# Performance work log

Measured on AMD Instinct MI355X. Metric: run time of the kernel, lower is better.

The kernel has to match this reference:

```python
import jax, jax.numpy as jnp
import numpy as np

SINKHORN_ITERS = 8
TEMPERATURE = 1.0
EPS = 1e-6


def sinkhorn(t):
    # log-domain Sinkhorn normalization, matching torch: log(clamp(t, min=eps)) / temp
    t = jnp.log(jnp.clip(t, EPS)) / TEMPERATURE
    for _ in range(SINKHORN_ITERS):
        t = t - jax.nn.logsumexp(t, axis=-2, keepdims=True)  # over tokens n
        t = t - jax.nn.logsumexp(t, axis=-1, keepdims=True)  # over experts e
    return jnp.exp(t)


def setup_inputs() -> dict:
    key = jax.random.key(0)
    k1, k2, k3 = jax.random.split(key, 3)
    B, N, D, E = 4, 4096, 1024, 8
    x = jax.random.normal(k1, (B, N, D), dtype=jnp.float32)
    gate_w = jax.random.normal(k2, (D, E), dtype=jnp.float32) * (D ** -0.5)
    experts = jax.random.normal(k3, (E, D, D), dtype=jnp.float32) * (D ** -0.5)
    return {"x": x, "gate_w": gate_w, "experts": experts}


def reference(x, gate_w, experts):
    B, N, D = x.shape
    E = gate_w.shape[-1]
    M = N // E  # tokens per expert

    gate_logits = jnp.einsum('bnd,de->bne', x, gate_w)
    competitive_gates = sinkhorn(gate_logits)  # b n e

    # topk along token dim (-2): transpose to (b,e,n), top_k along last axis
    vals, idx = jax.lax.top_k(jnp.swapaxes(competitive_gates, -1, -2), M)  # b e m
    gate_values = jnp.swapaxes(vals, -1, -2)   # b m e
    routed_indices = jnp.swapaxes(idx, -1, -2)  # b m e (int32)

    b_idx = jnp.arange(B)[:, None, None]  # (b,1,1)
    routed = x[b_idx, routed_indices]     # b m e d
    routed = jnp.transpose(routed, (2, 0, 1, 3))  # e b m d

    outputs = jnp.einsum('ebmd,edf->ebmf', routed, experts)  # e b m d
    outputs = outputs * jnp.transpose(gate_values, (2, 0, 1))[..., None]  # * (e b m 1)

    vals_bmed = jnp.transpose(outputs, (1, 2, 0, 3))  # b m e d
    routed_back = jnp.zeros_like(x).at[b_idx, routed_indices].set(vals_bmed)
    return routed_back
```

## Files before the change

kernel.cpp:

```cpp
#include <hip/hip_runtime.h>
#include <hip/hip_bf16.h>
#include <stdint.h>

typedef short s16x8 __attribute__((ext_vector_type(8)));
typedef float f32x4 __attribute__((ext_vector_type(4)));
typedef unsigned short u16;
typedef unsigned int u32;
typedef unsigned long long u64;

__device__ __forceinline__ float bf2f(u16 v){
  union { u32 u; float f; } c; c.u = ((u32)v) << 16; return c.f;
}

__device__ __forceinline__ u16 f2bf(float f){
  u32 u = __float_as_uint(f);
  u32 r = (u + 0x7FFFu + ((u >> 16) & 1u)) >> 16;
  return (u16)r;
}

__device__ __forceinline__ uint4 pack8(float4 a, float4 b){
  union { uint4 v; u16 s[8]; } o;
  o.s[0]=f2bf(a.x); o.s[1]=f2bf(a.y); o.s[2]=f2bf(a.z); o.s[3]=f2bf(a.w);
  o.s[4]=f2bf(b.x); o.s[5]=f2bf(b.y); o.s[6]=f2bf(b.z); o.s[7]=f2bf(b.w);
  return o.v;
}

__device__ __forceinline__ void gll16(const u16* g, u16* l){
  __builtin_amdgcn_global_load_lds((const __attribute__((address_space(1))) u32*)g,
                                   (__attribute__((address_space(3))) u32*)l, 16, 0, 0);
}

__global__ __launch_bounds__(64) void k_detect(const u32* __restrict__ x, int* __restrict__ flag){
  int lane = threadIdx.x;
  int cnt = 0;
  for (int i = lane; i < 4096; i += 64){
    u32 w = x[i];
    int ex = (w >> 7) & 0xFF;
    cnt += (ex >= 140) ? 1 : 0;
  }
  #pragma unroll
  for (int off = 32; off; off >>= 1) cnt += __shfl_xor(cnt, off, 64);
  if (lane == 0) *flag = (cnt > 256) ? 1 : 0;
}

__global__ __launch_bounds__(1024) void k_logits_cvt(const void* __restrict__ xv,
                                                     const void* __restrict__ gwv,
                                                     const int* __restrict__ flag,
                                                     u16* __restrict__ xb,
                                                     float* __restrict__ gates,
                                                     int mode){
  __shared__ float4 gw_swz[2048];
  __shared__ float  wacc[16][8];
  int is_f32 = *flag;
  int tid = threadIdx.x;

  {
    int r = tid;
    float g0,g1,g2,g3,g4,g5,g6,g7;
    if (is_f32){
      const float* gw = (const float*)gwv + ((size_t)r << 3);
      float4 u = *(const float4*)gw;
      float4 v = *(const float4*)(gw + 4);
      g0=u.x; g1=u.y; g2=u.z; g3=u.w; g4=v.x; g5=v.y; g6=v.z; g7=v.w;
    } else {
      union { uint4 v; u16 s[8]; } wu;
      wu.v = *(const uint4*)((const u16*)gwv + ((size_t)r << 3));
      g0=bf2f(wu.s[0]); g1=bf2f(wu.s[1]); g2=bf2f(wu.s[2]); g3=bf2f(wu.s[3]);
      g4=bf2f(wu.s[4]); g5=bf2f(wu.s[5]); g6=bf2f(wu.s[6]); g7=bf2f(wu.s[7]);
    }
    int p = r >> 3, j = r & 7;
    gw_swz[(p << 4) + (((j << 1)    ) ^ (p & 15))] = make_float4(g0,g1,g2,g3);
    gw_swz[(p << 4) + (((j << 1) | 1) ^ (p & 15))] = make_float4(g4,g5,g6,g7);
  }

  int tl = tid >> 7, pos = tid & 127;
  size_t base = ((((size_t)blockIdx.x << 3) + tl) << 10) + ((size_t)pos << 3);
  float xf[8];
  if (is_f32){
    const float* xr = (const float*)xv + base;
    float4 u = *(const float4*)xr;
    float4 v = *(const float4*)(xr + 4);
    xf[0]=u.x; xf[1]=u.y; xf[2]=u.z; xf[3]=u.w;
    xf[4]=v.x; xf[5]=v.y; xf[6]=v.z; xf[7]=v.w;
    if (mode) *(uint4*)(xb + base) = pack8(u, v);
  } else {
    uint4 raw = *(const uint4*)((const u16*)xv + base);
    union { uint4 v; u16 s[8]; } xu; xu.v = raw;
    #pragma unroll
    for (int k = 0; k < 8; k++) xf[k] = bf2f(xu.s[k]);
    if (mode) *(uint4*)(xb + base) = raw;
  }
  __syncthreads();

  float a0=0,a1=0,a2=0,a3=0,a4=0,a5=0,a6=0,a7=0;
  #pragma unroll
  for (int j = 0; j < 8; j++){
    float4 wA = gw_swz[(pos << 4) + (((j << 1)    ) ^ (pos & 15))];
    float4 wB = gw_swz[(pos << 4) + (((j << 1) | 1) ^ (pos & 15))];
    float xv8 = xf[j];
    a0 += xv8*wA.x; a1 += xv8*wA.y; a2 += xv8*wA.z; a3 += xv8*wA.w;
    a4 += xv8*wB.x; a5 += xv8*wB.y; a6 += xv8*wB.z; a7 += xv8*wB.w;
  }
  int wave = tid >> 6, lane = tid & 63;
  int s1 = lane & 1;
  float k0 = s1 ? a4 : a0, g0 = s1 ? a0 : a4;
  float k1 = s1 ? a5 : a1, g1 = s1 ? a1 : a5;
  float k2 = s1 ? a6 : a2, g2 = s1 ? a2 : a6;
  float k3 = s1 ? a7 : a3, g3 = s1 ? a3 : a7;
  k0 += __shfl_xor(g0, 1, 64); k1 += __shfl_xor(g1, 1, 64);
  k2 += __shfl_xor(g2, 1, 64); k3 += __shfl_xor(g3, 1, 64);
  int s2 = (lane >> 1) & 1;
  float m0 = s2 ? k2 : k0, h0 = s2 ? k0 : k2;
  float m1 = s2 ? k3 : k1, h1 = s2 ? k1 : k3;
  m0 += __shfl_xor(h0, 2, 64); m1 += __shfl_xor(h1, 2, 64);
  int s3 = (lane >> 2) & 1;
  float r = s3 ? m1 : m0, h = s3 ? m0 : m1;
  r += __shfl_xor(h, 4, 64);
  r += __shfl_xor(r, 8, 64);
  r += __shfl_xor(r, 16, 64);
  r += __shfl_xor(r, 32, 64);
  if (lane < 8){
    int e = ((lane & 1) << 2) | (lane & 2) | ((lane >> 2) & 1);
    wacc[wave][e] = r;
  }
  __syncthreads();
  if (tid < 64){
    int tt = tid >> 3, e = tid & 7;
    float v = wacc[(tt << 1)][e] + wacc[(tt << 1) | 1][e];
    gates[((((size_t)blockIdx.x << 3) + tt) << 3) + e] = v;
  }
}

__global__ __launch_bounds__(1024) void k_sink_cover(float* __restrict__ gates,
                                                     const void* __restrict__ Wv,
                                                     const int* __restrict__ flag,
                                                     u16* __restrict__ WT,
                                                     uint4* __restrict__ out,
                                                     int out_size, int mode){
  __shared__ __align__(16) char smem[36864];
  int bx = blockIdx.x;
  int tid = threadIdx.x;

  if (bx < 4){
    float* wred = (float*)smem;
    float* lbc  = wred + 128;
    int wave = tid >> 6, lane = tid & 63;
    float* gb = gates + ((size_t)bx << 15);
    float4 va[4], vb[4];
    #pragma unroll
    for (int q = 0; q < 4; q++){
      float* gp = gb + (((q << 10) + tid) << 3);
      float4 a = *(const float4*)gp;
      float4 b = *(const float4*)(gp + 4);
      a.x=fmaxf(a.x,1e-6f); a.y=fmaxf(a.y,1e-6f); a.z=fmaxf(a.z,1e-6f); a.w=fmaxf(a.w,1e-6f);
      b.x=fmaxf(b.x,1e-6f); b.y=fmaxf(b.y,1e-6f); b.z=fmaxf(b.z,1e-6f); b.w=fmaxf(b.w,1e-6f);
      va[q]=a; vb[q]=b;
    }
    for (int it = 0; it < 8; it++){
      float s0 = ((va[0].x+va[1].x)+(va[2].x+va[3].x));
      float s1 = ((va[0].y+va[1].y)+(va[2].y+va[3].y));
      float s2 = ((va[0].z+va[1].z)+(va[2].z+va[3].z));
      float s3 = ((va[0].w+va[1].w)+(va[2].w+va[3].w));
      float s4 = ((vb[0].x+vb[1].x)+(vb[2].x+vb[3].x));
      float s5 = ((vb[0].y+vb[1].y)+(vb[2].y+vb[3].y));
      float s6 = ((vb[0].z+vb[1].z)+(vb[2].z+vb[3].z));
      float s7 = ((vb[0].w+vb[1].w)+(vb[2].w+vb[3].w));
      #pragma unroll
      for (int off = 32; off; off >>= 1){
        s0 += __shfl_xor(s0, off, 64); s1 += __shfl_xor(s1, off, 64);
        s2 += __shfl_xor(s2, off, 64); s3 += __shfl_xor(s3, off, 64);
        s4 += __shfl_xor(s4, off, 64); s5 += __shfl_xor(s5, off, 64);
        s6 += __shfl_xor(s6, off, 64); s7 += __shfl_xor(s7, off, 64);
      }
      if (lane == 0){
        wred[(wave<<3)+0]=s0; wred[(wave<<3)+1]=s1; wred[(wave<<3)+2]=s2; wred[(wave<<3)+3]=s3;
        wred[(wave<<3)+4]=s4; wred[(wave<<3)+5]=s5; wred[(wave<<3)+6]=s6; wred[(wave<<3)+7]=s7;
      }
      __syncthreads();
      if (tid < 8){
        float S = 0.f;
        #pragma unroll
        for (int w2 = 0; w2 < 16; w2++) S += wred[(w2 << 3) + tid];
        lbc[tid] = 1.0f / S;
      }
      __syncthreads();
      float i0=lbc[0], i1=lbc[1], i2=lbc[2], i3=lbc[3];
      float i4=lbc[4], i5=lbc[5], i6=lbc[6], i7=lbc[7];
      #pragma unroll
      for (int q = 0; q < 4; q++){
        float4 a = va[q], b = vb[q];
        a.x*=i0; a.y*=i1; a.z*=i2; a.w*=i3;
        b.x*=i4; b.y*=i5; b.z*=i6; b.w*=i7;
        float rs = ((a.x+a.y)+(a.z+a.w)) + ((b.x+b.y)+(b.z+b.w));
        float ir = 1.0f / rs;
        a.x*=ir; a.y*=ir; a.z*=ir; a.w*=ir;
        b.x*=ir; b.y*=ir; b.z*=ir; b.w*=ir;
        va[q]=a; vb[q]=b;
      }
    }
    #pragma unroll
    for (int q = 0; q < 4; q++){
      float* gp = gb + (((q << 10) + tid) << 3);
      *(float4*)gp = va[q];
      *(float4*)(gp + 4) = vb[q];
    }
    return;
  }

  if (mode == 0){
    int is_f32 = *flag;
    int rb = bx - 4;
    size_t words = (size_t)out_size >> (is_f32 ? 0 : 1);
    size_t n4 = words >> 2;
    size_t i = (size_t)rb * 1024 + tid;
    uint4 z = make_uint4(0, 0, 0, 0);
    for (; i < n4; i += (size_t)512 * 1024) out[i] = z;
    return;
  }

  if (bx < 516){
    int is_f32 = *flag;
    int rb = bx - 4;
    int sub = tid >> 8;
    int t = tid & 255;
    int g = (rb << 2) + sub;
    int e = g >> 8, t2 = g & 255;
    int td = (t2 >> 4) << 6, tf = (t2 & 15) << 6;
    u16 (*tile)[72] = (u16(*)[72])(smem + (size_t)sub * (64 * 72 * 2));
    #pragma unroll
    for (int i = 0; i < 2; i++){
      int id = t + (i << 8);
      int row = id >> 3, c8 = id & 7;
      size_t src = ((size_t)(e*1024 + td + row))*1024 + tf + (c8 << 3);
      uint4 v;
      if (is_f32){
        const float* wf = (const float*)Wv;
        v = pack8(*(const float4*)(wf + src), *(const float4*)(wf + src + 4));
      } else {
        v = *(const uint4*)((const u16*)Wv + src);
      }
      *(uint4*)&tile[row][c8 << 3] = v;
    }
    __syncthreads();
    #pragma unroll
    for (int i = 0; i < 2; i++){
      int id = t + (i << 8);
      int frow = id >> 3, c8 = id & 7;
      union { uint4 v; u16 s[8]; } o;
      #pragma unroll
      for (int j = 0; j < 8; j++) o.s[j] = tile[(c8 << 3) + j][frow];
      *(uint4*)(WT + ((size_t)(e*1024 + tf + frow))*1024 + td + (c8 << 3)) = o.v;
    }
    return;
  }

  {
    int is_f32 = *flag;
    int rb = bx - 516;
    size_t words = (size_t)out_size >> (is_f32 ? 0 : 1);
    size_t n4 = words >> 2;
    size_t i = (size_t)rb * 1024 + tid;
    uint4 z = make_uint4(0, 0, 0, 0);
    for (; i < n4; i += (size_t)512 * 1024) out[i] = z;
  }
}

__global__ __launch_bounds__(256) void k_rank(const float* __restrict__ gates,
                                              int* __restrict__ routed, int* __restrict__ winner){
  __shared__ u32 ord_s[4096];
  __shared__ u32 cnt_s[1024];
  int bx = blockIdx.x;
  int be = bx >> 5;
  int b = be >> 3, e = be & 7;
  int slice = bx & 31;
  int tid = threadIdx.x;
  const float* gb = gates + (size_t)b * (4096 * 8);
  for (int i = tid; i < 4096; i += 256){
    float v = gb[(i << 3) + e];
    u32 fb = __float_as_uint(v);
    ord_s[i] = fb ^ ((fb >> 31) ? 0xFFFFFFFFu : 0x80000000u);
  }
  __syncthreads();

  int tg = tid & 31;
  int js = tid >> 5;
  int i0 = (slice << 7) + (tg << 2);
  int gchunk = i0 & ~7;
  u32 v0 = ord_s[i0], v1 = ord_s[i0+1], v2 = ord_s[i0+2], v3 = ord_s[i0+3];
  int jlo = js << 9, jhi = jlo + 512;
  int c0 = 0, c1 = 0, c2 = 0, c3 = 0;

  int endA = min(jhi, gchunk);
  for (int j = jlo; j < endA; j += 8){
    uint4 w0 = *(const uint4*)&ord_s[j];
    uint4 w1 = *(const uint4*)&ord_s[j + 4];
    c0 += (w0.x>=v0)+(w0.y>=v0)+(w0.z>=v0)+(w0.w>=v0)+(w1.x>=v0)+(w1.y>=v0)+(w1.z>=v0)+(w1.w>=v0);
    c1 += (w0.x>=v1)+(w0.y>=v1)+(w0.z>=v1)+(w0.w>=v1)+(w1.x>=v1)+(w1.y>=v1)+(w1.z>=v1)+(w1.w>=v1);
    c2 += (w0.x>=v2)+(w0.y>=v2)+(w0.z>=v2)+(w0.w>=v2)+(w1.x>=v2)+(w1.y>=v2)+(w1.z>=v2)+(w1.w>=v2);
    c3 += (w0.x>=v3)+(w0.y>=v3)+(w0.z>=v3)+(w0.w>=v3)+(w1.x>=v3)+(w1.y>=v3)+(w1.z>=v3)+(w1.w>=v3);
  }
  int begB = max(jlo, gchunk + 8);
  for (int j = begB; j < jhi; j += 8){
    uint4 w0 = *(const uint4*)&ord_s[j];
    uint4 w1 = *(const uint4*)&ord_s[j + 4];
    c0 += (w0.x>v0)+(w0.y>v0)+(w0.z>v0)+(w0.w>v0)+(w1.x>v0)+(w1.y>v0)+(w1.z>v0)+(w1.w>v0);
    c1 += (w0.x>v1)+(w0.y>v1)+(w0.z>v1)+(w0.w>v1)+(w1.x>v1)+(w1.y>v1)+(w1.z>v1)+(w1.w>v1);
    c2 += (w0.x>v2)+(w0.y>v2)+(w0.z>v2)+(w0.w>v2)+(w1.x>v2)+(w1.y>v2)+(w1.z>v2)+(w1.w>v2);
    c3 += (w0.x>v3)+(w0.y>v3)+(w0.z>v3)+(w0.w>v3)+(w1.x>v3)+(w1.y>v3)+(w1.z>v3)+(w1.w>v3);
  }
  if (gchunk >= jlo && gchunk < jhi){
    int base_off = i0 & 7;
    #pragma unroll
    for (int jj = 0; jj < 8; jj++){
      u32 w = ord_s[gchunk + jj];
      c0 += (jj < base_off + 0) ? (w >= v0) : (w > v0);
      c1 += (jj < base_off + 1) ? (w >= v1) : (w > v1);
      c2 += (jj < base_off + 2) ? (w >= v2) : (w > v2);
      c3 += (jj < base_off + 3) ? (w >= v3) : (w > v3);
    }
  }
  int lt = tg << 2;
  cnt_s[(js << 7) + lt + 0] = c0;
  cnt_s[(js << 7) + lt + 1] = c1;
  cnt_s[(js << 7) + lt + 2] = c2;
  cnt_s[(js << 7) + lt + 3] = c3;
  __syncthreads();
  if (tid < 128){
    int rank = 0;
    #pragma unroll
    for (int s = 0; s < 8; s++) rank += cnt_s[(s << 7) + tid];
    int i = (slice << 7) + tid;
    if (rank < 512){
      routed[(be << 9) + rank] = i;
      atomicMax(&winner[(b << 12) + i], (rank << 3) | e);
    }
  }
}

__global__ __launch_bounds__(256) void k_gemm_fast(const u16* __restrict__ xb, const u16* __restrict__ WT,
                                                   const float* __restrict__ gates,
                                                   const int* __restrict__ routed,
                                                   const int* __restrict__ winner,
                                                   const int* __restrict__ flag,
                                                   void* __restrict__ outv){
  __shared__ u16 As[128 * 32];
  __shared__ u16 Bs[128 * 32];
  __shared__ int   tok_s[128];
  __shared__ float gate_s[128];
  __shared__ int   flg_s[128];
  int is_f32 = *flag;
  int bx = blockIdx.x;
  int e = bx & 7;
  int rest = bx >> 3;
  int b = rest >> 5;
  int tile = rest & 31;
  int mt = tile & 3, nt = tile >> 2;
  int tid = threadIdx.x;
  int w = tid >> 6, lane = tid & 63;
  int quad = lane >> 4, l16 = lane & 15;

  const int* idx_base = routed + (((b << 3) + e) << 9) + (mt << 7);

  if (tid < 128){
    int tok = idx_base[tid];
    int mg  = (mt << 7) + tid;
    int win = winner[(b << 12) + tok];
    tok_s[tid]  = tok;
    flg_s[tid]  = (win == ((mg << 3) | e)) ? 1 : 0;
    gate_s[tid] = gates[((((size_t)b << 12) + tok) << 3) + e];
  }
  __syncthreads();

  int r0 = tid >> 2;
  int ch = tid & 3;
  int r1 = r0 + 64;
  int swz = ch ^ ((r0 >> 1) & 3);
  const u16* gA0 = xb + ((((size_t)b << 12) + tok_s[r0]) << 10) + (swz << 3);
  const u16* gA1 = xb + ((((size_t)b << 12) + tok_s[r1]) << 10) + (swz << 3);
  int f0 = nt << 7;
  const u16* gB0 = WT + ((((size_t)e << 10) + f0 + r0) << 10) + (swz << 3);
  const u16* gB1 = WT + ((((size_t)e << 10) + f0 + r1) << 10) + (swz << 3);
  u16* lA0 = As + (w << 9);
  u16* lA1 = As + 2048 + (w << 9);
  u16* lB0 = Bs + (w << 9);
  u16* lB1 = Bs + 2048 + (w << 9);
  int swzr = quad ^ ((l16 >> 1) & 3);

  f32x4 acc[4][4] = {};
  int wm = (w & 1) << 6, wn = (w >> 1) << 6;

  for (int k0 = 0; k0 < 1024; k0 += 32){
    gll16(gA0 + k0, lA0);
    gll16(gA1 + k0, lA1);
    gll16(gB0 + k0, lB0);
    gll16(gB1 + k0, lB1);
    __syncthreads();
    s16x8 af[4], bv[4];
    #pragma unroll
    for (int im = 0; im < 4; im++)
      af[im] = *(const s16x8*)&As[((wm + (im << 4) + l16) << 5) + (swzr << 3)];
    #pragma unroll
    for (int in = 0; in < 4; in++)
      bv[in] = *(const s16x8*)&Bs[((wn + (in << 4) + l16) << 5) + (swzr << 3)];
    __syncthreads();
    #pragma unroll
    for (int im = 0; im < 4; im++){
      #pragma unroll
      for (int in = 0; in < 4; in++)
        acc[im][in] = __builtin_amdgcn_mfma_f32_16x16x32_bf16(af[im], bv[in], acc[im][in], 0, 0, 0);
    }
  }

  #pragma unroll
  for (int im = 0; im < 4; im++){
    #pragma unroll
    for (int r = 0; r < 4; r++){
      int mrow = wm + (im << 4) + (quad << 2) + r;
      if (flg_s[mrow]){
        float g  = gate_s[mrow];
        int tok  = tok_s[mrow];
        size_t obase = ((((size_t)b << 12) + tok) << 10) + f0 + wn + l16;
        if (is_f32){
          float* o32 = (float*)outv;
          #pragma unroll
          for (int in = 0; in < 4; in++) o32[obase + (in << 4)] = acc[im][in][r] * g;
        } else {
          u16* o16 = (u16*)outv;
          #pragma unroll
          for (int in = 0; in < 4; in++) o16[obase + (in << 4)] = f2bf(acc[im][in][r] * g);
        }
      }
    }
  }
}

__global__ __launch_bounds__(256) void k_gemm_slow(const void* __restrict__ xv, const void* __restrict__ Wv,
                                                   const float* __restrict__ gates,
                                                   const int* __restrict__ routed,
                                                   const int* __restrict__ winner,
                                                   const int* __restrict__ flag,
                                                   void* __restrict__ outv){
  __shared__ u16 As[128 * 32];
  __shared__ u16 Bw[32 * 132];
  __shared__ u16 Bs[128 * 32];
  __shared__ int   tok_s[128];
  __shared__ float gate_s[128];
  __shared__ int   flg_s[128];
  int is_f32 = *flag;
  int bx = blockIdx.x;
  int e = bx & 7;
  int rest = bx >> 3;
  int b = rest >> 5;
  int tile = rest & 31;
  int mt = tile & 3, nt = tile >> 2;
  int tid = threadIdx.x;
  int w = tid >> 6, lane = tid & 63;
  int quad = lane >> 4, l16 = lane & 15;

  const int* idx_base = routed + (((b << 3) + e) << 9) + (mt << 7);

  if (tid < 128){
    int tok = idx_base[tid];
    int mg  = (mt << 7) + tid;
    int win = winner[(b << 12) + tok];
    tok_s[tid]  = tok;
    flg_s[tid]  = (win == ((mg << 3) | e)) ? 1 : 0;
    gate_s[tid] = gates[((((size_t)b << 12) + tok) << 3) + e];
  }
  __syncthreads();

  int r0 = tid >> 2;
  int ch = tid & 3;
  int r1 = r0 + 64;
  size_t offA0 = ((((size_t)b << 12) + tok_s[r0]) << 10) + (ch << 3);
  size_t offA1 = ((((size_t)b << 12) + tok_s[r1]) << 10) + (ch << 3);
  int f0 = nt << 7;
  int kkB0 = tid >> 4;
  int fcB  = tid & 15;
  size_t offB0 = ((size_t)e << 20) + ((size_t)kkB0 << 10) + f0 + (fcB << 3);
  size_t offB1 = offB0 + ((size_t)16 << 10);
  int f_loc = tid >> 1;
  int half  = tid & 1;

  f32x4 acc[4][4] = {};
  int wm = (w & 1) << 6, wn = (w >> 1) << 6;

  for (int k0 = 0; k0 < 1024; k0 += 32){
    uint4 a0, a1, b0, b1;
    if (is_f32){
      const float* xf = (const float*)xv;
      const float* wf = (const float*)Wv;
      a0 = pack8(*(const float4*)(xf + offA0 + k0), *(const float4*)(xf + offA0 + k0 + 4));
      a1 = pack8(*(const float4*)(xf + offA1 + k0), *(const float4*)(xf + offA1 + k0 + 4));
      b0 = pack8(*(const float4*)(wf + offB0 + ((size_t)k0 << 10)),
                 *(const float4*)(wf + offB0 + ((size_t)k0 << 10) + 4));
      b1 = pack8(*(const float4*)(wf + offB1 + ((size_t)k0 << 10)),
                 *(const float4*)(wf + offB1 + ((size_t)k0 << 10) + 4));
    } else {
      const u16* xh = (const u16*)xv;
      const u16* wh = (const u16*)Wv;
      a0 = *(const uint4*)(xh + offA0 + k0);
      a1 = *(const uint4*)(xh + offA1 + k0);
      b0 = *(const uint4*)(wh + offB0 + ((size_t)k0 << 10));
      b1 = *(const uint4*)(wh + offB1 + ((size_t)k0 << 10));
    }
    *(uint4*)&As[(r0 << 5) + (ch << 3)] = a0;
    *(uint4*)&As[(r1 << 5) + (ch << 3)] = a1;
    *(uint4*)&Bw[kkB0 * 132 + (fcB << 3)] = b0;
    *(uint4*)&Bw[(kkB0 + 16) * 132 + (fcB << 3)] = b1;
    __syncthreads();
    union { uint4 v[2]; u16 s[16]; } tv;
    #pragma unroll
    for (int j = 0; j < 16; j++) tv.s[j] = Bw[((half << 4) + j) * 132 + f_loc];
    *(uint4*)&Bs[(f_loc << 5) + (half << 4)]     = tv.v[0];
    *(uint4*)&Bs[(f_loc << 5) + (half << 4) + 8] = tv.v[1];
    __syncthreads();
    s16x8 af[4], bv[4];
    #pragma unroll
    for (int im = 0; im < 4; im++)
      af[im] = *(const s16x8*)&As[((wm + (im << 4) + l16) << 5) + (quad << 3)];
    #pragma unroll
    for (int in = 0; in < 4; in++)
      bv[in] = *(const s16x8*)&Bs[((wn + (in << 4) + l16) << 5) + (quad << 3)];
    __syncthreads();
    #pragma unroll
    for (int im = 0; im < 4; im++){
      #pragma unroll
      for (int in = 0; in < 4; in++)
        acc[im][in] = __builtin_amdgcn_mfma_f32_16x16x32_bf16(af[im], bv[in], acc[im][in], 0, 0, 0);
    }
  }

  #pragma unroll
  for (int im = 0; im < 4; im++){
    #pragma unroll
    for (int r = 0; r < 4; r++){
      int mrow = wm + (im << 4) + (quad << 2) + r;
      if (flg_s[mrow]){
        float g  = gate_s[mrow];
        int tok  = tok_s[mrow];
        size_t obase = ((((size_t)b << 12) + tok) << 10) + f0 + wn + l16;
        if (is_f32){
          float* o32 = (float*)outv;
          #pragma unroll
          for (int in = 0; in < 4; in++) o32[obase + (in << 4)] = acc[im][in][r] * g;
        } else {
          u16* o16 = (u16*)outv;
          #pragma unroll
          for (int in = 0; in < 4; in++) o16[obase + (in << 4)] = f2bf(acc[im][in][r] * g);
        }
      }
    }
  }
}

extern "C" void kernel_launch(void* const* d_in, const int* in_sizes, int n_in,
                              void* d_out, int out_size, void* d_ws, size_t ws_size,
                              hipStream_t stream){
  const void* x  = d_in[0];
  const void* gw = d_in[1];
  const void* W  = d_in[2];
  char* ws = (char*)d_ws;
  float* gates  = (float*)ws;
  int*   winner = (int*)(ws + 524288);
  int*   routed = (int*)(ws + 589824);
  int*   flag   = (int*)(ws + 655360);
  u16*   xb     = (u16*)(ws + 655616);
  u16*   WT     = (u16*)(ws + 655616 + 33554432);
  size_t need_fast = 655616ull + 33554432ull + 16777216ull;
  bool fast = ws_size >= need_fast;

  hipMemsetAsync(winner, 0xFF, 65536, stream);
  hipLaunchKernelGGL(k_detect, dim3(1), dim3(64), 0, stream, (const u32*)x, flag);
  hipLaunchKernelGGL(k_logits_cvt, dim3(2048), dim3(1024), 0, stream,
                     x, gw, flag, xb, gates, fast ? 1 : 0);
  if (fast){
    hipLaunchKernelGGL(k_sink_cover, dim3(1028), dim3(1024), 0, stream,
                       gates, W, flag, WT, (uint4*)d_out, out_size, 1);
    hipLaunchKernelGGL(k_rank, dim3(1024), dim3(256), 0, stream, gates, routed, winner);
    hipLaunchKernelGGL(k_gemm_fast, dim3(1024), dim3(256), 0, stream, xb, WT, gates, routed, winner,
                       flag, d_out);
  } else {
    hipLaunchKernelGGL(k_sink_cover, dim3(516), dim3(1024), 0, stream,
                       gates, W, flag, WT, (uint4*)d_out, out_size, 0);
    hipLaunchKernelGGL(k_rank, dim3(1024), dim3(256), 0, stream, gates, routed, winner);
    hipLaunchKernelGGL(k_gemm_slow, dim3(1024), dim3(256), 0, stream, x, W, gates, routed, winner,
                       flag, d_out);
  }
}
```

Baseline: 276.4 us.

## Double-buffer GEMM LDS tiles and fold winner memset into logits kernel

The expert GEMM main loop now uses two LDS buffers, so the global-to-LDS loads for the next K-slice are issued before the MFMAs on the current one, with a single waitcnt+barrier per stage instead of two barriers. Separately, the hipMemsetAsync that initialised the winner array is removed and done by the first 16 blocks of the logits kernel, saving one launch. The double buffer doubles LDS use per block, which may lower occupancy, and the vmcnt(0) wait still serialises each stage somewhat.

```diff
diff --git a/kernel.cpp b/kernel.cpp
--- a/kernel.cpp
+++ b/kernel.cpp
@@ -48,11 +48,14 @@
                                                      const int* __restrict__ flag,
                                                      u16* __restrict__ xb,
                                                      float* __restrict__ gates,
+                                                     int* __restrict__ winner,
                                                      int mode){
   __shared__ float4 gw_swz[2048];
   __shared__ float  wacc[16][8];
   int is_f32 = *flag;
   int tid = threadIdx.x;
+
+  if (blockIdx.x < 16) winner[(blockIdx.x << 10) + tid] = -1;
 
   {
     int r = tid;
@@ -343,8 +346,8 @@
                                                    const int* __restrict__ winner,
                                                    const int* __restrict__ flag,
                                                    void* __restrict__ outv){
-  __shared__ u16 As[128 * 32];
-  __shared__ u16 Bs[128 * 32];
+  __shared__ u16 As[2][4096];
+  __shared__ u16 Bs[2][4096];
   __shared__ int   tok_s[128];
   __shared__ float gate_s[128];
   __shared__ int   flg_s[128];
@@ -380,36 +383,55 @@
   int f0 = nt << 7;
   const u16* gB0 = WT + ((((size_t)e << 10) + f0 + r0) << 10) + (swz << 3);
   const u16* gB1 = WT + ((((size_t)e << 10) + f0 + r1) << 10) + (swz << 3);
-  u16* lA0 = As + (w << 9);
-  u16* lA1 = As + 2048 + (w << 9);
-  u16* lB0 = Bs + (w << 9);
-  u16* lB1 = Bs + 2048 + (w << 9);
+  int wbase = w << 9;
   int swzr = quad ^ ((l16 >> 1) & 3);
 
   f32x4 acc[4][4] = {};
   int wm = (w & 1) << 6, wn = (w >> 1) << 6;
 
-  for (int k0 = 0; k0 < 1024; k0 += 32){
-    gll16(gA0 + k0, lA0);
-    gll16(gA1 + k0, lA1);
-    gll16(gB0 + k0, lB0);
-    gll16(gB1 + k0, lB1);
-    __syncthreads();
-    s16x8 af[4], bv[4];
-    #pragma unroll
-    for (int im = 0; im < 4; im++)
-      af[im] = *(const s16x8*)&As[((wm + (im << 4) + l16) << 5) + (swzr << 3)];
-    #pragma unroll
-    for (int in = 0; in < 4; in++)
-      bv[in] = *(const s16x8*)&Bs[((wn + (in << 4) + l16) << 5) + (swzr << 3)];
-    __syncthreads();
-    #pragma unroll
-    for (int im = 0; im < 4; im++){
-      #pragma unroll
-      for (int in = 0; in < 4; in++)
-        acc[im][in] = __builtin_amdgcn_mfma_f32_16x16x32_bf16(af[im], bv[in], acc[im][in], 0, 0, 0);
-    }
-  }
+#define STAGE(d, K)  do { \
+    gll16(gA0 + (K), &As[d][wbase]); \
+    gll16(gA1 + (K), &As[d][2048 + wbase]); \
+    gll16(gB0 + (K), &Bs[d][wbase]); \
+    gll16(gB1 + (K), &Bs[d][2048 + wbase]); \
+  } while (0)
+
+#define COMPUTE(d)  do { \
+    s16x8 af[4], bv[4]; \
+    _Pragma("unroll") \
+    for (int im = 0; im < 4; im++) \
+      af[im] = *(const s16x8*)&As[d][((wm + (im << 4) + l16) << 5) + (swzr << 3)]; \
+    _Pragma("unroll") \
+    for (int in = 0; in < 4; in++) \
+      bv[in] = *(const s16x8*)&Bs[d][((wn + (in << 4) + l16) << 5) + (swzr << 3)]; \
+    _Pragma("unroll") \
+    for (int im = 0; im < 4; im++){ \
+      _Pragma("unroll") \
+      for (int in = 0; in < 4; in++) \
+        acc[im][in] = __builtin_amdgcn_mfma_f32_16x16x32_bf16(af[im], bv[in], acc[im][in], 0, 0, 0); \
+    } \
+  } while (0)
+
+#define PIPE_BAR()  do { \
+    asm volatile("s_waitcnt vmcnt(0)" ::: "memory"); \
+    __builtin_amdgcn_sched_barrier(0); \
+    __builtin_amdgcn_s_barrier(); \
+  } while (0)
+
+  STAGE(0, 0);
+  PIPE_BAR();
+  #pragma unroll 1
+  for (int k0 = 0; k0 < 1024; k0 += 64){
+    STAGE(1, k0 + 32);
+    COMPUTE(0);
+    PIPE_BAR();
+    if (k0 + 64 < 1024) STAGE(0, k0 + 64);
+    COMPUTE(1);
+    PIPE_BAR();
+  }
+#undef STAGE
+#undef COMPUTE
+#undef PIPE_BAR
 
   #pragma unroll
   for (int im = 0; im < 4; im++){
@@ -570,10 +592,9 @@
   size_t need_fast = 655616ull + 33554432ull + 16777216ull;
   bool fast = ws_size >= need_fast;
 
-  hipMemsetAsync(winner, 0xFF, 65536, stream);
   hipLaunchKernelGGL(k_detect, dim3(1), dim3(64), 0, stream, (const u32*)x, flag);
   hipLaunchKernelGGL(k_logits_cvt, dim3(2048), dim3(1024), 0, stream,
-                     x, gw, flag, xb, gates, fast ? 1 : 0);
+                     x, gw, flag, xb, gates, winner, fast ? 1 : 0);
   if (fast){
     hipLaunchKernelGGL(k_sink_cover, dim3(1028), dim3(1024), 0, stream,
                        gates, W, flag, WT, (uint4*)d_out, out_size, 1);
```

Result: no change. 276.6 us (+0.1%).

## Merge prep kernels, split Sinkhorn out, zero only unrouted output rows in GEMM

Applied to the files above, without the earlier changes.

Replaces the memset, detect kernel and logits kernel with one prep kernel. Every block recomputes the dtype detection and the winner array is initialised inside the same kernel, while the expert-weight transpose runs in the same grid. Sinkhorn moves into its own 4-block kernel, so it no longer shares a launch with the weight transpose. The full-output zero fill is dropped; extra GEMM blocks zero only the rows no expert won, which cuts output write traffic. The costs are redundant detection reads in every block, and the slow path no longer clears the output unless the mode==0 branch still handles it.

```diff
diff --git a/kernel.cpp b/kernel.cpp
--- a/kernel.cpp
+++ b/kernel.cpp
@@ -30,186 +30,124 @@
                                    (__attribute__((address_space(3))) u32*)l, 16, 0, 0);
 }
 
-__global__ __launch_bounds__(64) void k_detect(const u32* __restrict__ x, int* __restrict__ flag){
-  int lane = threadIdx.x;
-  int cnt = 0;
-  for (int i = lane; i < 4096; i += 64){
-    u32 w = x[i];
-    int ex = (w >> 7) & 0xFF;
-    cnt += (ex >= 140) ? 1 : 0;
-  }
-  #pragma unroll
-  for (int off = 32; off; off >>= 1) cnt += __shfl_xor(cnt, off, 64);
-  if (lane == 0) *flag = (cnt > 256) ? 1 : 0;
-}
-
-__global__ __launch_bounds__(1024) void k_logits_cvt(const void* __restrict__ xv,
-                                                     const void* __restrict__ gwv,
-                                                     const int* __restrict__ flag,
-                                                     u16* __restrict__ xb,
-                                                     float* __restrict__ gates,
-                                                     int mode){
-  __shared__ float4 gw_swz[2048];
-  __shared__ float  wacc[16][8];
-  int is_f32 = *flag;
-  int tid = threadIdx.x;
-
-  {
-    int r = tid;
-    float g0,g1,g2,g3,g4,g5,g6,g7;
-    if (is_f32){
-      const float* gw = (const float*)gwv + ((size_t)r << 3);
-      float4 u = *(const float4*)gw;
-      float4 v = *(const float4*)(gw + 4);
-      g0=u.x; g1=u.y; g2=u.z; g3=u.w; g4=v.x; g5=v.y; g6=v.z; g7=v.w;
-    } else {
-      union { uint4 v; u16 s[8]; } wu;
-      wu.v = *(const uint4*)((const u16*)gwv + ((size_t)r << 3));
-      g0=bf2f(wu.s[0]); g1=bf2f(wu.s[1]); g2=bf2f(wu.s[2]); g3=bf2f(wu.s[3]);
-      g4=bf2f(wu.s[4]); g5=bf2f(wu.s[5]); g6=bf2f(wu.s[6]); g7=bf2f(wu.s[7]);
-    }
-    int p = r >> 3, j = r & 7;
-    gw_swz[(p << 4) + (((j << 1)    ) ^ (p & 15))] = make_float4(g0,g1,g2,g3);
-    gw_swz[(p << 4) + (((j << 1) | 1) ^ (p & 15))] = make_float4(g4,g5,g6,g7);
-  }
-
-  int tl = tid >> 7, pos = tid & 127;
-  size_t base = ((((size_t)blockIdx.x << 3) + tl) << 10) + ((size_t)pos << 3);
-  float xf[8];
-  if (is_f32){
-    const float* xr = (const float*)xv + base;
-    float4 u = *(const float4*)xr;
-    float4 v = *(const float4*)(xr + 4);
-    xf[0]=u.x; xf[1]=u.y; xf[2]=u.z; xf[3]=u.w;
-    xf[4]=v.x; xf[5]=v.y; xf[6]=v.z; xf[7]=v.w;
-    if (mode) *(uint4*)(xb + base) = pack8(u, v);
-  } else {
-    uint4 raw = *(const uint4*)((const u16*)xv + base);
-    union { uint4 v; u16 s[8]; } xu; xu.v = raw;
-    #pragma unroll
-    for (int k = 0; k < 8; k++) xf[k] = bf2f(xu.s[k]);
-    if (mode) *(uint4*)(xb + base) = raw;
-  }
-  __syncthreads();
-
-  float a0=0,a1=0,a2=0,a3=0,a4=0,a5=0,a6=0,a7=0;
-  #pragma unroll
-  for (int j = 0; j < 8; j++){
-    float4 wA = gw_swz[(pos << 4) + (((j << 1)    ) ^ (pos & 15))];
-    float4 wB = gw_swz[(pos << 4) + (((j << 1) | 1) ^ (pos & 15))];
-    float xv8 = xf[j];
-    a0 += xv8*wA.x; a1 += xv8*wA.y; a2 += xv8*wA.z; a3 += xv8*wA.w;
-    a4 += xv8*wB.x; a5 += xv8*wB.y; a6 += xv8*wB.z; a7 += xv8*wB.w;
-  }
-  int wave = tid >> 6, lane = tid & 63;
-  int s1 = lane & 1;
-  float k0 = s1 ? a4 : a0, g0 = s1 ? a0 : a4;
-  float k1 = s1 ? a5 : a1, g1 = s1 ? a1 : a5;
-  float k2 = s1 ? a6 : a2, g2 = s1 ? a2 : a6;
-  float k3 = s1 ? a7 : a3, g3 = s1 ? a3 : a7;
-  k0 += __shfl_xor(g0, 1, 64); k1 += __shfl_xor(g1, 1, 64);
-  k2 += __shfl_xor(g2, 1, 64); k3 += __shfl_xor(g3, 1, 64);
-  int s2 = (lane >> 1) & 1;
-  float m0 = s2 ? k2 : k0, h0 = s2 ? k0 : k2;
-  float m1 = s2 ? k3 : k1, h1 = s2 ? k1 : k3;
-  m0 += __shfl_xor(h0, 2, 64); m1 += __shfl_xor(h1, 2, 64);
-  int s3 = (lane >> 2) & 1;
-  float r = s3 ? m1 : m0, h = s3 ? m0 : m1;
-  r += __shfl_xor(h, 4, 64);
-  r += __shfl_xor(r, 8, 64);
-  r += __shfl_xor(r, 16, 64);
-  r += __shfl_xor(r, 32, 64);
-  if (lane < 8){
-    int e = ((lane & 1) << 2) | (lane & 2) | ((lane >> 2) & 1);
-    wacc[wave][e] = r;
-  }
-  __syncthreads();
-  if (tid < 64){
-    int tt = tid >> 3, e = tid & 7;
-    float v = wacc[(tt << 1)][e] + wacc[(tt << 1) | 1][e];
-    gates[((((size_t)blockIdx.x << 3) + tt) << 3) + e] = v;
-  }
-}
-
-__global__ __launch_bounds__(1024) void k_sink_cover(float* __restrict__ gates,
-                                                     const void* __restrict__ Wv,
-                                                     const int* __restrict__ flag,
-                                                     u16* __restrict__ WT,
-                                                     uint4* __restrict__ out,
-                                                     int out_size, int mode){
+__global__ __launch_bounds__(1024) void k_prep(const void* __restrict__ xv,
+                                               const void* __restrict__ gwv,
+                                               const void* __restrict__ Wv,
+                                               u16* __restrict__ xb,
+                                               u16* __restrict__ WT,
+                                               float* __restrict__ gates,
+                                               int* __restrict__ winner,
+                                               int* __restrict__ flag,
+                                               uint4* __restrict__ out,
+                                               int out_size, int mode){
   __shared__ __align__(16) char smem[36864];
+  __shared__ float wacc[16][8];
+  __shared__ int   dred[16];
   int bx = blockIdx.x;
   int tid = threadIdx.x;
-
-  if (bx < 4){
-    float* wred = (float*)smem;
-    float* lbc  = wred + 128;
-    int wave = tid >> 6, lane = tid & 63;
-    float* gb = gates + ((size_t)bx << 15);
-    float4 va[4], vb[4];
-    #pragma unroll
-    for (int q = 0; q < 4; q++){
-      float* gp = gb + (((q << 10) + tid) << 3);
-      float4 a = *(const float4*)gp;
-      float4 b = *(const float4*)(gp + 4);
-      a.x=fmaxf(a.x,1e-6f); a.y=fmaxf(a.y,1e-6f); a.z=fmaxf(a.z,1e-6f); a.w=fmaxf(a.w,1e-6f);
-      b.x=fmaxf(b.x,1e-6f); b.y=fmaxf(b.y,1e-6f); b.z=fmaxf(b.z,1e-6f); b.w=fmaxf(b.w,1e-6f);
-      va[q]=a; vb[q]=b;
-    }
-    for (int it = 0; it < 8; it++){
-      float s0 = ((va[0].x+va[1].x)+(va[2].x+va[3].x));
-      float s1 = ((va[0].y+va[1].y)+(va[2].y+va[3].y));
-      float s2 = ((va[0].z+va[1].z)+(va[2].z+va[3].z));
-      float s3 = ((va[0].w+va[1].w)+(va[2].w+va[3].w));
-      float s4 = ((vb[0].x+vb[1].x)+(vb[2].x+vb[3].x));
-      float s5 = ((vb[0].y+vb[1].y)+(vb[2].y+vb[3].y));
-      float s6 = ((vb[0].z+vb[1].z)+(vb[2].z+vb[3].z));
-      float s7 = ((vb[0].w+vb[1].w)+(vb[2].w+vb[3].w));
+  int wave = tid >> 6, lane = tid & 63;
+
+  int cnt = 0;
+  {
+    const u32* xw = (const u32*)xv;
+    #pragma unroll
+    for (int i = 0; i < 4; i++){
+      u32 w = xw[(i << 10) + tid];
+      cnt += (((w >> 7) & 0xFF) >= 140) ? 1 : 0;
+    }
+    #pragma unroll
+    for (int off = 32; off; off >>= 1) cnt += __shfl_xor(cnt, off, 64);
+    if (lane == 0) dred[wave] = cnt;
+  }
+  __syncthreads();
+  int tot = 0;
+  #pragma unroll
+  for (int w2 = 0; w2 < 16; w2++) tot += dred[w2];
+  int is_f32 = (tot > 256) ? 1 : 0;
+  if (bx == 0 && tid == 0) *flag = is_f32;
+
+  if (bx < 2048){
+    if (bx < 16) winner[(bx << 10) + tid] = -1;
+    float4* gw_swz = (float4*)smem;
+    {
+      int r = tid;
+      float g0,g1,g2,g3,g4,g5,g6,g7;
+      if (is_f32){
+        const float* gw = (const float*)gwv + ((size_t)r << 3);
+        float4 u = *(const float4*)gw;
+        float4 v = *(const float4*)(gw + 4);
+        g0=u.x; g1=u.y; g2=u.z; g3=u.w; g4=v.x; g5=v.y; g6=v.z; g7=v.w;
+      } else {
+        union { uint4 v; u16 s[8]; } wu;
+        wu.v = *(const uint4*)((const u16*)gwv + ((size_t)r << 3));
+        g0=bf2f(wu.s[0]); g1=bf2f(wu.s[1]); g2=bf2f(wu.s[2]); g3=bf2f(wu.s[3]);
+        g4=bf2f(wu.s[4]); g5=bf2f(wu.s[5]); g6=bf2f(wu.s[6]); g7=bf2f(wu.s[7]);
+      }
+      int p = r >> 3, j = r & 7;
+      gw_swz[(p << 4) + (((j << 1)    ) ^ (p & 15))] = make_float4(g0,g1,g2,g3);
+      gw_swz[(p << 4) + (((j << 1) | 1) ^ (p & 15))] = make_float4(g4,g5,g6,g7);
+    }
+
+    int tl = tid >> 7, pos = tid & 127;
+    size_t base = ((((size_t)bx << 3) + tl) << 10) + ((size_t)pos << 3);
+    float xf[8];
+    if (is_f32){
+      const float* xr = (const float*)xv + base;
+      float4 u = *(const float4*)xr;
+      float4 v = *(const float4*)(xr + 4);
+      xf[0]=u.x; xf[1]=u.y; xf[2]=u.z; xf[3]=u.w;
+      xf[4]=v.x; xf[5]=v.y; xf[6]=v.z; xf[7]=v.w;
+      if (mode) *(uint4*)(xb + base) = pack8(u, v);
+    } else {
+      uint4 raw = *(const uint4*)((const u16*)xv + base);
+      union { uint4 v; u16 s[8]; } xu; xu.v = raw;
       #pragma unroll
-      for (int off = 32; off; off >>= 1){
-        s0 += __shfl_xor(s0, off, 64); s1 += __shfl_xor(s1, off, 64);
-        s2 += __shfl_xor(s2, off, 64); s3 += __shfl_xor(s3, off, 64);
-        s4 += __shfl_xor(s4, off, 64); s5 += __shfl_xor(s5, off, 64);
-        s6 += __shfl_xor(s6, off, 64); s7 += __shfl_xor(s7, off, 64);
-      }
-      if (lane == 0){
-        wred[(wave<<3)+0]=s0; wred[(wave<<3)+1]=s1; wred[(wave<<3)+2]=s2; wred[(wave<<3)+3]=s3;
-        wred[(wave<<3)+4]=s4; wred[(wave<<3)+5]=s5; wred[(wave<<3)+6]=s6; wred[(wave<<3)+7]=s7;
-      }
-      __syncthreads();
-      if (tid < 8){
-        float S = 0.f;
-        #pragma unroll
-        for (int w2 = 0; w2 < 16; w2++) S += wred[(w2 << 3) + tid];
-        lbc[tid] = 1.0f / S;
-      }
-      __syncthreads();
-      float i0=lbc[0], i1=lbc[1], i2=lbc[2], i3=lbc[3];
-      float i4=lbc[4], i5=lbc[5], i6=lbc[6], i7=lbc[7];
-      #pragma unroll
-      for (int q = 0; q < 4; q++){
-        float4 a = va[q], b = vb[q];
-        a.x*=i0; a.y*=i1; a.z*=i2; a.w*=i3;
-        b.x*=i4; b.y*=i5; b.z*=i6; b.w*=i7;
-        float rs = ((a.x+a.y)+(a.z+a.w)) + ((b.x+b.y)+(b.z+b.w));
-        float ir = 1.0f / rs;
-        a.x*=ir; a.y*=ir; a.z*=ir; a.w*=ir;
-        b.x*=ir; b.y*=ir; b.z*=ir; b.w*=ir;
-        va[q]=a; vb[q]=b;
-      }
-    }
-    #pragma unroll
-    for (int q = 0; q < 4; q++){
-      float* gp = gb + (((q << 10) + tid) << 3);
-      *(float4*)gp = va[q];
-      *(float4*)(gp + 4) = vb[q];
+      for (int k = 0; k < 8; k++) xf[k] = bf2f(xu.s[k]);
+      if (mode) *(uint4*)(xb + base) = raw;
+    }
+    __syncthreads();
+
+    float a0=0,a1=0,a2=0,a3=0,a4=0,a5=0,a6=0,a7=0;
+    #pragma unroll
+    for (int j = 0; j < 8; j++){
+      float4 wA = gw_swz[(pos << 4) + (((j << 1)    ) ^ (pos & 15))];
+      float4 wB = gw_swz[(pos << 4) + (((j << 1) | 1) ^ (pos & 15))];
+      float xv8 = xf[j];
+      a0 += xv8*wA.x; a1 += xv8*wA.y; a2 += xv8*wA.z; a3 += xv8*wA.w;
+      a4 += xv8*wB.x; a5 += xv8*wB.y; a6 += xv8*wB.z; a7 += xv8*wB.w;
+    }
+    int s1 = lane & 1;
+    float k0 = s1 ? a4 : a0, g0 = s1 ? a0 : a4;
+    float k1 = s1 ? a5 : a1, g1 = s1 ? a1 : a5;
+    float k2 = s1 ? a6 : a2, g2 = s1 ? a2 : a6;
+    float k3 = s1 ? a7 : a3, g3 = s1 ? a3 : a7;
+    k0 += __shfl_xor(g0, 1, 64); k1 += __shfl_xor(g1, 1, 64);
+    k2 += __shfl_xor(g2, 1, 64); k3 += __shfl_xor(g3, 1, 64);
+    int s2 = (lane >> 1) & 1;
+    float m0 = s2 ? k2 : k0, h0 = s2 ? k0 : k2;
+    float m1 = s2 ? k3 : k1, h1 = s2 ? k1 : k3;
+    m0 += __shfl_xor(h0, 2, 64); m1 += __shfl_xor(h1, 2, 64);
+    int s3 = (lane >> 2) & 1;
+    float r = s3 ? m1 : m0, h = s3 ? m0 : m1;
+    r += __shfl_xor(h, 4, 64);
+    r += __shfl_xor(r, 8, 64);
+    r += __shfl_xor(r, 16, 64);
+    r += __shfl_xor(r, 32, 64);
+    if (lane < 8){
+      int e = ((lane & 1) << 2) | (lane & 2) | ((lane >> 2) & 1);
+      wacc[wave][e] = r;
+    }
+    __syncthreads();
+    if (tid < 64){
+      int tt = tid >> 3, e = tid & 7;
+      float v = wacc[(tt << 1)][e] + wacc[(tt << 1) | 1][e];
+      gates[((((size_t)bx << 3) + tt) << 3) + e] = v;
     }
     return;
   }
 
   if (mode == 0){
-    int is_f32 = *flag;
-    int rb = bx - 4;
+    int rb = bx - 2048;
     size_t words = (size_t)out_size >> (is_f32 ? 0 : 1);
     size_t n4 = words >> 2;
     size_t i = (size_t)rb * 1024 + tid;
@@ -218,9 +156,8 @@
     return;
   }
 
-  if (bx < 516){
-    int is_f32 = *flag;
-    int rb = bx - 4;
+  {
+    int rb = bx - 2048;
     int sub = tid >> 8;
     int t = tid & 255;
     int g = (rb << 2) + sub;
@@ -251,17 +188,73 @@
       for (int j = 0; j < 8; j++) o.s[j] = tile[(c8 << 3) + j][frow];
       *(uint4*)(WT + ((size_t)(e*1024 + tf + frow))*1024 + td + (c8 << 3)) = o.v;
     }
-    return;
-  }
-
-  {
-    int is_f32 = *flag;
-    int rb = bx - 516;
-    size_t words = (size_t)out_size >> (is_f32 ? 0 : 1);
-    size_t n4 = words >> 2;
-    size_t i = (size_t)rb * 1024 + tid;
-    uint4 z = make_uint4(0, 0, 0, 0);
-    for (; i < n4; i += (size_t)512 * 1024) out[i] = z;
+  }
+}
+
+__global__ __launch_bounds__(1024) void k_sinkhorn(float* __restrict__ gates){
+  __shared__ float wred[128];
+  __shared__ float lbc[8];
+  int bx = blockIdx.x;
+  int tid = threadIdx.x;
+  int wave = tid >> 6, lane = tid & 63;
+  float* gb = gates + ((size_t)bx << 15);
+  float4 va[4], vb[4];
+  #pragma unroll
+  for (int q = 0; q < 4; q++){
+    float* gp = gb + (((q << 10) + tid) << 3);
+    float4 a = *(const float4*)gp;
+    float4 b = *(const float4*)(gp + 4);
+    a.x=fmaxf(a.x,1e-6f); a.y=fmaxf(a.y,1e-6f); a.z=fmaxf(a.z,1e-6f); a.w=fmaxf(a.w,1e-6f);
+    b.x=fmaxf(b.x,1e-6f); b.y=fmaxf(b.y,1e-6f); b.z=fmaxf(b.z,1e-6f); b.w=fmaxf(b.w,1e-6f);
+    va[q]=a; vb[q]=b;
+  }
+  for (int it = 0; it < 8; it++){
+    float s0 = ((va[0].x+va[1].x)+(va[2].x+va[3].x));
+    float s1 = ((va[0].y+va[1].y)+(va[2].y+va[3].y));
+    float s2 = ((va[0].z+va[1].z)+(va[2].z+va[3].z));
+    float s3 = ((va[0].w+va[1].w)+(va[2].w+va[3].w));
+    float s4 = ((vb[0].x+vb[1].x)+(vb[2].x+vb[3].x));
+    float s5 = ((vb[0].y+vb[1].y)+(vb[2].y+vb[3].y));
+    float s6 = ((vb[0].z+vb[1].z)+(vb[2].z+vb[3].z));
+    float s7 = ((vb[0].w+vb[1].w)+(vb[2].w+vb[3].w));
+    #pragma unroll
+    for (int off = 32; off; off >>= 1){
+      s0 += __shfl_xor(s0, off, 64); s1 += __shfl_xor(s1, off, 64);
+      s2 += __shfl_xor(s2, off, 64); s3 += __shfl_xor(s3, off, 64);
+      s4 += __shfl_xor(s4, off, 64); s5 += __shfl_xor(s5, off, 64);
+      s6 += __shfl_xor(s6, off, 64); s7 += __shfl_xor(s7, off, 64);
+    }
+    if (lane == 0){
+      wred[(wave<<3)+0]=s0; wred[(wave<<3)+1]=s1; wred[(wave<<3)+2]=s2; wred[(wave<<3)+3]=s3;
+      wred[(wave<<3)+4]=s4; wred[(wave<<3)+5]=s5; wred[(wave<<3)+6]=s6; wred[(wave<<3)+7]=s7;
+    }
+    __syncthreads();
+    if (tid < 8){
+      float S = 0.f;
+      #pragma unroll
+      for (int w2 = 0; w2 < 16; w2++) S += wred[(w2 << 3) + tid];
+      lbc[tid] = 1.0f / S;
+    }
+    __syncthreads();
+    float i0=lbc[0], i1=lbc[1], i2=lbc[2], i3=lbc[3];
+    float i4=lbc[4], i5=lbc[5], i6=lbc[6], i7=lbc[7];
+    #pragma unroll
+    for (int q = 0; q < 4; q++){
+      float4 a = va[q], b = vb[q];
+      a.x*=i0; a.y*=i1; a.z*=i2; a.w*=i3;
+      b.x*=i4; b.y*=i5; b.z*=i6; b.w*=i7;
+      float rs = ((a.x+a.y)+(a.z+a.w)) + ((b.x+b.y)+(b.z+b.w));
+      float ir = 1.0f / rs;
+      a.x*=ir; a.y*=ir; a.z*=ir; a.w*=ir;
+      b.x*=ir; b.y*=ir; b.z*=ir; b.w*=ir;
+      va[q]=a; vb[q]=b;
+    }
+  }
+  #pragma unroll
+  for (int q = 0; q < 4; q++){
+    float* gp = gb + (((q << 10) + tid) << 3);
+    *(float4*)gp = va[q];
+    *(float4*)(gp + 4) = vb[q];
   }
 }
 
@@ -350,12 +343,33 @@
   __shared__ int   flg_s[128];
   int is_f32 = *flag;
   int bx = blockIdx.x;
+  int tid = threadIdx.x;
+
+  if (bx >= 1024){
+    int zb = bx - 1024;
+    #pragma unroll 1
+    for (int i = 0; i < 128; i++){
+      int g = (zb << 7) + i;
+      if (winner[g] < 0){
+        size_t rbase = ((size_t)g) << 10;
+        if (is_f32){
+          float* o = (float*)outv;
+          *(float4*)(o + rbase + (tid << 2)) = make_float4(0.f, 0.f, 0.f, 0.f);
+        } else {
+          u16* o = (u16*)outv;
+          uint2 z; z.x = 0; z.y = 0;
+          *(uint2*)(o + rbase + (tid << 2)) = z;
+        }
+      }
+    }
+    return;
+  }
+
   int e = bx & 7;
   int rest = bx >> 3;
   int b = rest >> 5;
   int tile = rest & 31;
   int mt = tile & 3, nt = tile >> 2;
-  int tid = threadIdx.x;
   int w = tid >> 6, lane = tid & 63;
   int quad = lane >> 4, l16 = lane & 15;
 
@@ -570,20 +584,15 @@
   size_t need_fast = 655616ull + 33554432ull + 16777216ull;
   bool fast = ws_size >= need_fast;
 
-  hipMemsetAsync(winner, 0xFF, 65536, stream);
-  hipLaunchKernelGGL(k_detect, dim3(1), dim3(64), 0, stream, (const u32*)x, flag);
-  hipLaunchKernelGGL(k_logits_cvt, dim3(2048), dim3(1024), 0, stream,
-                     x, gw, flag, xb, gates, fast ? 1 : 0);
+  hipLaunchKernelGGL(k_prep, dim3(2560), dim3(1024), 0, stream,
+                     x, gw, W, xb, WT, gates, winner, flag, (uint4*)d_out, out_size,
+                     fast ? 1 : 0);
+  hipLaunchKernelGGL(k_sinkhorn, dim3(4), dim3(1024), 0, stream, gates);
+  hipLaunchKernelGGL(k_rank, dim3(1024), dim3(256), 0, stream, gates, routed, winner);
   if (fast){
-    hipLaunchKernelGGL(k_sink_cover, dim3(1028), dim3(1024), 0, stream,
-                       gates, W, flag, WT, (uint4*)d_out, out_size, 1);
-    hipLaunchKernelGGL(k_rank, dim3(1024), dim3(256), 0, stream, gates, routed, winner);
-    hipLaunchKernelGGL(k_gemm_fast, dim3(1024), dim3(256), 0, stream, xb, WT, gates, routed, winner,
+    hipLaunchKernelGGL(k_gemm_fast, dim3(1152), dim3(256), 0, stream, xb, WT, gates, routed, winner,
                        flag, d_out);
   } else {
-    hipLaunchKernelGGL(k_sink_cover, dim3(516), dim3(1024), 0, stream,
-                       gates, W, flag, WT, (uint4*)d_out, out_size, 0);
-    hipLaunchKernelGGL(k_rank, dim3(1024), dim3(256), 0, stream, gates, routed, winner);
     hipLaunchKernelGGL(k_gemm_slow, dim3(1024), dim3(256), 0, stream, x, W, gates, routed, winner,
                        flag, d_out);
   }
```

New measurement: 276.9 us. About the same (+0.2%).
